# Kernel tuning notes

Hardware: AMD Instinct MI355X
Metric: run time of the kernel (lower is better)

The kernel has to match this reference:

```python
import jax, jax.numpy as jnp
import numpy as np

N = 100000
E = 3200000
NFEAT = 256
NHID = 128
NCLASS = 40
SCALE = 1.0


def setup_inputs() -> dict:
    key = jax.random.key(0)
    ks = jax.random.split(key, 8)
    x = jax.random.normal(ks[0], (N, NFEAT), dtype=jnp.float32)
    adj_row = jnp.sort(jax.random.randint(ks[1], (E,), 0, N, dtype=jnp.int32))
    adj_col = jax.random.randint(ks[2], (E,), 0, N, dtype=jnp.int32)
    adj_val = jax.random.uniform(ks[3], (E,), dtype=jnp.float32)
    # parameters (reset_parameters: weight ~ N(0,1), bias ~ N(-1,1) -> normal with mean -1? no:
    # bias.normal_(-stdv, stdv) with stdv=1 means mean=-1, std=1)
    W1 = jax.random.normal(ks[4], (NFEAT, NHID), dtype=jnp.float32)
    b1 = jax.random.normal(ks[5], (NHID,), dtype=jnp.float32) - 1.0
    W2 = jax.random.normal(ks[6], (NHID, NCLASS), dtype=jnp.float32)
    b2 = jax.random.normal(ks[7], (NCLASS,), dtype=jnp.float32) - 1.0
    return {"x": x, "adj_row": adj_row, "adj_col": adj_col, "adj_val": adj_val,
            "i": 0, "W1": W1, "b1": b1, "W2": W2, "b2": b2}


def spmm(row, col, val, dense):
    # adj @ dense where adj is sparse COO [N, N]
    gathered = val[:, None] * dense[col]          # [E, D]
    return jax.ops.segment_sum(gathered, row, num_segments=N)


def reference(x, adj_row, adj_col, adj_val, i, W1, b1, W2, b2):
    # layer 1: support = x @ W1; out = adj @ support + b1
    h = spmm(adj_row, adj_col, adj_val, x @ W1) + b1
    h = jax.nn.relu(h) * SCALE
    # dropout is identity (eval mode / training=False)
    # layer 2
    logits = spmm(adj_row, adj_col, adj_val, h @ W2) + b2
    return jax.nn.log_softmax(logits, axis=1)
```

## Files before the change

### kernel.cpp

```cpp
#include <hip/hip_runtime.h>
#include <hip/hip_bf16.h>
#include <math.h>


#define GCN_NFEAT 256
#define GCN_NHID  128
#define GCN_NCLASS 40

typedef __bf16 bf16_t;
typedef bf16_t bf16x8 __attribute__((ext_vector_type(8)));
typedef float  f32x4  __attribute__((ext_vector_type(4)));

static __device__ __forceinline__ unsigned short f2b(float f) {
    bf16_t b = (bf16_t)f;
    return *(unsigned short*)&b;
}
static __device__ __forceinline__ float blo(unsigned int u) {
    return __uint_as_float(u << 16);
}
static __device__ __forceinline__ float bhi(unsigned int u) {
    return __uint_as_float(u & 0xffff0000u);
}

__global__ __launch_bounds__(256) void k_row_ptr(
    const int* __restrict__ row, int* __restrict__ row_ptr, int n_rows, int n_edges)
{
    int r = blockIdx.x * blockDim.x + threadIdx.x;
    if (r > n_rows) return;
    int lo = 0, hi = n_edges;
    while (lo < hi) {
        int mid = (lo + hi) >> 1;
        if (row[mid] < r) lo = mid + 1; else hi = mid;
    }
    row_ptr[r] = lo;
}

__global__ __launch_bounds__(256) void k_prep_w1t(
    const float* __restrict__ w1, bf16_t* __restrict__ w1t)
{
    int idx = blockIdx.x * 256 + threadIdx.x;
    int c = idx & 127;
    int k = idx >> 7;
    w1t[(size_t)c * GCN_NFEAT + k] = (bf16_t)w1[(size_t)k * GCN_NHID + c];
}

__global__ __launch_bounds__(256) void k_prep_w2t(
    const float* __restrict__ w2, bf16_t* __restrict__ w2t)
{
    int idx = blockIdx.x * 256 + threadIdx.x;
    if (idx >= 48 * GCN_NHID) return;
    int c = idx / GCN_NHID;
    int k = idx - c * GCN_NHID;
    float v = (c < GCN_NCLASS) ? w2[(size_t)k * GCN_NCLASS + c] : 0.f;
    w2t[idx] = (bf16_t)v;
}

__global__ __launch_bounds__(256) void k_gemm1(
    const float* __restrict__ x, const bf16_t* __restrict__ w1t,
    bf16_t* __restrict__ out, int nrows)
{
    __shared__ __align__(16) bf16_t As[128][72];
    __shared__ __align__(16) bf16_t Bs[128][72];

    const int tid  = threadIdx.x;
    const int wave = tid >> 6, lane = tid & 63;
    const int wm = wave >> 1, wn = wave & 1;
    const int lm = lane & 15, quad = lane >> 4;
    const int r0 = blockIdx.x * 128;

    f32x4 acc[4][4] = {};

    for (int k0 = 0; k0 < GCN_NFEAT; k0 += 64) {
        {
            const int row = tid >> 1, half = tid & 1;
            const int gr = r0 + row;
            union { bf16_t b[32]; uint4 q[4]; } t;
            if (gr < nrows) {
                const float* p = x + (size_t)gr * GCN_NFEAT + k0 + half * 32;
#pragma unroll
                for (int i = 0; i < 8; i++) {
                    float4 v = ((const float4*)p)[i];
                    t.b[i*4+0] = (bf16_t)v.x; t.b[i*4+1] = (bf16_t)v.y;
                    t.b[i*4+2] = (bf16_t)v.z; t.b[i*4+3] = (bf16_t)v.w;
                }
            } else {
#pragma unroll
                for (int i = 0; i < 4; i++) t.q[i] = make_uint4(0,0,0,0);
            }
            uint4* dst = (uint4*)&As[row][half * 32];
#pragma unroll
            for (int i = 0; i < 4; i++) dst[i] = t.q[i];
        }
        {
            const int colc = tid >> 1, half = tid & 1;
            const uint4* src = (const uint4*)(w1t + (size_t)colc * GCN_NFEAT + k0 + half * 32);
            uint4* dst = (uint4*)&Bs[colc][half * 32];
#pragma unroll
            for (int i = 0; i < 4; i++) dst[i] = src[i];
        }
        __syncthreads();

#pragma unroll
        for (int ks = 0; ks < 2; ks++) {
            bf16x8 af[4], bfr[4];
#pragma unroll
            for (int i = 0; i < 4; i++)
                af[i] = *(const bf16x8*)&As[wm*64 + i*16 + lm][ks*32 + quad*8];
#pragma unroll
            for (int j = 0; j < 4; j++)
                bfr[j] = *(const bf16x8*)&Bs[wn*64 + j*16 + lm][ks*32 + quad*8];
#pragma unroll
            for (int i = 0; i < 4; i++)
#pragma unroll
                for (int j = 0; j < 4; j++)
                    acc[i][j] = __builtin_amdgcn_mfma_f32_16x16x32_bf16(
                        af[i], bfr[j], acc[i][j], 0, 0, 0);
        }
        __syncthreads();
    }

#pragma unroll
    for (int i = 0; i < 4; i++) {
#pragma unroll
        for (int reg = 0; reg < 4; reg++) {
            const int gr = r0 + wm*64 + i*16 + quad*4 + reg;
            if (gr < nrows) {
#pragma unroll
                for (int j = 0; j < 4; j++) {
                    const int gc = wn*64 + j*16 + lm;
                    out[(size_t)gr * GCN_NHID + gc] = (bf16_t)acc[i][j][reg];
                }
            }
        }
    }
}

__global__ __launch_bounds__(256) void k_spmm1(
    const int* __restrict__ row_ptr, const int* __restrict__ col,
    const float* __restrict__ val, const unsigned int* __restrict__ sup,
    const float* __restrict__ b1, unsigned int* __restrict__ h, int nrows)
{
    const int wid  = (blockIdx.x * blockDim.x + threadIdx.x) >> 6;
    const int lane = threadIdx.x & 63;
    if (wid >= nrows) return;
    const int e0 = row_ptr[wid];
    const int e1 = row_ptr[wid + 1];
    const int sub = lane & 15;

    float ax = 0.f, ay = 0.f;
    int e = e0;
    for (; e + 16 <= e1; e += 16) {
        const int   cv = col[e + sub];
        const float vv = val[e + sub];
#pragma unroll
        for (int j = 0; j < 16; j++) {
            const int   cj = __shfl(cv, j, 64);
            const float vj = __shfl(vv, j, 64);
            const unsigned int u = sup[(unsigned)(cj << 6) + lane];
            ax = fmaf(vj, blo(u), ax);
            ay = fmaf(vj, bhi(u), ay);
        }
    }
    for (; e < e1; e++) {
        const int c = col[e];
        const float v = val[e];
        const unsigned int u = sup[(unsigned)(c << 6) + lane];
        ax = fmaf(v, blo(u), ax);
        ay = fmaf(v, bhi(u), ay);
    }

    const float2 bb = *(const float2*)(b1 + lane * 2);
    const float ox = fmaxf(ax + bb.x, 0.f);
    const float oy = fmaxf(ay + bb.y, 0.f);
    h[(unsigned)(wid << 6) + lane] = (unsigned int)f2b(ox) | ((unsigned int)f2b(oy) << 16);
}

__global__ __launch_bounds__(256) void k_gemm2(
    const bf16_t* __restrict__ h, const bf16_t* __restrict__ w2t,
    bf16_t* __restrict__ out, int nrows)
{
    __shared__ __align__(16) bf16_t As[128][136];
    __shared__ __align__(16) bf16_t Bs[48][136];

    const int tid  = threadIdx.x;
    const int wave = tid >> 6, lane = tid & 63;
    const int lm = lane & 15, quad = lane >> 4;
    const int r0 = blockIdx.x * 128;

    {
        const int row = tid >> 1, half = tid & 1;
        const int gr = r0 + row;
        uint4* dst = (uint4*)&As[row][half * 64];
        if (gr < nrows) {
            const uint4* src = (const uint4*)(h + (size_t)gr * GCN_NHID + half * 64);
#pragma unroll
            for (int i = 0; i < 8; i++) dst[i] = src[i];
        } else {
#pragma unroll
            for (int i = 0; i < 8; i++) dst[i] = make_uint4(0,0,0,0);
        }
    }
    for (int idx = tid; idx < 48 * 16; idx += 256) {
        const int c = idx >> 4, seg = idx & 15;
        ((uint4*)&Bs[c][0])[seg] = ((const uint4*)(w2t + (size_t)c * GCN_NHID))[seg];
    }
    __syncthreads();

    f32x4 acc[2][3] = {};
#pragma unroll
    for (int ks = 0; ks < 4; ks++) {
        bf16x8 af[2], bfr[3];
#pragma unroll
        for (int i = 0; i < 2; i++)
            af[i] = *(const bf16x8*)&As[wave*32 + i*16 + lm][ks*32 + quad*8];
#pragma unroll
        for (int j = 0; j < 3; j++)
            bfr[j] = *(const bf16x8*)&Bs[j*16 + lm][ks*32 + quad*8];
#pragma unroll
        for (int i = 0; i < 2; i++)
#pragma unroll
            for (int j = 0; j < 3; j++)
                acc[i][j] = __builtin_amdgcn_mfma_f32_16x16x32_bf16(
                    af[i], bfr[j], acc[i][j], 0, 0, 0);
    }

#pragma unroll
    for (int i = 0; i < 2; i++) {
#pragma unroll
        for (int reg = 0; reg < 4; reg++) {
            const int gr = r0 + wave*32 + i*16 + quad*4 + reg;
            if (gr < nrows) {
#pragma unroll
                for (int j = 0; j < 3; j++) {
                    const int gc = j*16 + lm;
                    if (gc < GCN_NCLASS)
                        out[(size_t)gr * GCN_NCLASS + gc] = (bf16_t)acc[i][j][reg];
                }
            }
        }
    }
}

__global__ __launch_bounds__(256) void k_spmm2_lsm(
    const int* __restrict__ row_ptr, const int* __restrict__ col,
    const float* __restrict__ val, const unsigned int* __restrict__ sup2,
    const float* __restrict__ b2, float* __restrict__ out, int nrows)
{
    const int wid  = (blockIdx.x * blockDim.x + threadIdx.x) >> 6;
    const int lane = threadIdx.x & 63;
    const int g    = lane / 20;
    const int li   = lane - g * 20;
    const int r    = wid * 3 + g;
    const bool active = (g < 3) && (r < nrows);

    int e0 = 0, e1 = 0;
    if (active) { e0 = row_ptr[r]; e1 = row_ptr[r + 1]; }

    float ax = 0.f, ay = 0.f;
    int e = e0;
    for (; e + 3 < e1; e += 4) {
        const int c0 = col[e],   c1 = col[e+1], c2 = col[e+2], c3 = col[e+3];
        const float v0 = val[e], v1 = val[e+1], v2 = val[e+2], v3 = val[e+3];
        const unsigned int u0 = sup2[(unsigned)(c0 * 20) + li];
        const unsigned int u1 = sup2[(unsigned)(c1 * 20) + li];
        const unsigned int u2 = sup2[(unsigned)(c2 * 20) + li];
        const unsigned int u3 = sup2[(unsigned)(c3 * 20) + li];
        ax = fmaf(v0, blo(u0), ax); ay = fmaf(v0, bhi(u0), ay);
        ax = fmaf(v1, blo(u1), ax); ay = fmaf(v1, bhi(u1), ay);
        ax = fmaf(v2, blo(u2), ax); ay = fmaf(v2, bhi(u2), ay);
        ax = fmaf(v3, blo(u3), ax); ay = fmaf(v3, bhi(u3), ay);
    }
    for (; e < e1; e++) {
        const unsigned int u = sup2[(unsigned)(col[e] * 20) + li];
        const float v = val[e];
        ax = fmaf(v, blo(u), ax); ay = fmaf(v, bhi(u), ay);
    }

    float l0 = -INFINITY, l1 = -INFINITY;
    if (active) {
        l0 = ax + b2[li * 2];
        l1 = ay + b2[li * 2 + 1];
    }

    float m = fmaxf(l0, l1);
#pragma unroll
    for (int off = 16; off >= 1; off >>= 1) {
        const float t = __shfl_down(m, off, 64);
        if (li + off < 20) m = fmaxf(m, t);
    }
    m = __shfl(m, g * 20, 64);

    float s = active ? (__expf(l0 - m) + __expf(l1 - m)) : 0.f;
#pragma unroll
    for (int off = 16; off >= 1; off >>= 1) {
        const float t = __shfl_down(s, off, 64);
        if (li + off < 20) s += t;
    }
    s = __shfl(s, g * 20, 64);

    if (active) {
        const float lse = m + __logf(s);
        float* p = out + (size_t)r * GCN_NCLASS + li * 2;
        p[0] = l0 - lse;
        p[1] = l1 - lse;
    }
}

extern "C" void kernel_launch(void* const* d_in, const int* in_sizes, int n_in,
                              void* d_out, int out_size, void* d_ws, size_t ws_size,
                              hipStream_t stream)
{
    const float* x       = (const float*)d_in[0];
    const int*   adj_row = (const int*)  d_in[1];
    const int*   adj_col = (const int*)  d_in[2];
    const float* adj_val = (const float*)d_in[3];
    const float* W1 = (const float*)d_in[5];
    const float* b1 = (const float*)d_in[6];
    const float* W2 = (const float*)d_in[7];
    const float* b2 = (const float*)d_in[8];
    float* out = (float*)d_out;

    const int N = in_sizes[0] / GCN_NFEAT;
    const int E = in_sizes[1];

    char* ws = (char*)d_ws;
    size_t off = 0;
    int* row_ptr = (int*)(ws + off);
    off += (((size_t)(N + 1) * sizeof(int)) + 1023) & ~(size_t)1023;
    bf16_t* w1t = (bf16_t*)(ws + off);
    off += ((size_t)GCN_NHID * GCN_NFEAT * 2 + 1023) & ~(size_t)1023;
    bf16_t* w2t = (bf16_t*)(ws + off);
    off += ((size_t)48 * GCN_NHID * 2 + 1023) & ~(size_t)1023;
    bf16_t* sup1 = (bf16_t*)(ws + off);
    off += ((size_t)N * GCN_NHID * 2 + 1023) & ~(size_t)1023;
    bf16_t* h = (bf16_t*)(ws + off);
    bf16_t* sup2 = sup1;

    k_row_ptr<<<(N + 1 + 255) / 256, 256, 0, stream>>>(adj_row, row_ptr, N, E);
    k_prep_w1t<<<GCN_NHID * GCN_NFEAT / 256, 256, 0, stream>>>(W1, w1t);
    k_prep_w2t<<<(48 * GCN_NHID + 255) / 256, 256, 0, stream>>>(W2, w2t);
    k_gemm1<<<(N + 127) / 128, 256, 0, stream>>>(x, w1t, sup1, N);
    k_spmm1<<<(N + 3) / 4, 256, 0, stream>>>(row_ptr, adj_col, adj_val,
                                             (const unsigned int*)sup1, b1,
                                             (unsigned int*)h, N);
    k_gemm2<<<(N + 127) / 128, 256, 0, stream>>>(h, w2t, sup2, N);
    const int nw2 = (N + 2) / 3;
    k_spmm2_lsm<<<(nw2 + 3) / 4, 256, 0, stream>>>(row_ptr, adj_col, adj_val,
                                                   (const unsigned int*)sup2, b2, out, N);
}
```

Before: 417.3 us.

## Merge prep kernels, use 16-byte gathers in spmm1, add nontemporal loads

Merges the row-pointer and weight-transpose launches into one kernel. Rewrites spmm1 so each wave handles four edges at once: each 16-lane quarter gathers a full 256-byte bf16 row with 16-byte loads, and partial sums are combined with cross-lane shuffles. Adds nontemporal loads for x in gemm1 and for col/val in the spmm kernels, and an 8-way unrolled loop in spmm2. The aim is to cut launch overhead and gather instruction count and to improve memory-level parallelism, at the cost of extra shuffle reductions and more complex tail handling.

Measured after the change: 426.0 us. 1.02x slower.

```diff
diff --git a/kernel.cpp b/kernel.cpp
--- a/kernel.cpp
+++ b/kernel.cpp
@@ -10,6 +10,7 @@
 typedef __bf16 bf16_t;
 typedef bf16_t bf16x8 __attribute__((ext_vector_type(8)));
 typedef float  f32x4  __attribute__((ext_vector_type(4)));
+typedef float  f32x4e __attribute__((ext_vector_type(4)));
 
 static __device__ __forceinline__ unsigned short f2b(float f) {
     bf16_t b = (bf16_t)f;
@@ -22,37 +23,35 @@
     return __uint_as_float(u & 0xffff0000u);
 }
 
-__global__ __launch_bounds__(256) void k_row_ptr(
-    const int* __restrict__ row, int* __restrict__ row_ptr, int n_rows, int n_edges)
-{
-    int r = blockIdx.x * blockDim.x + threadIdx.x;
-    if (r > n_rows) return;
-    int lo = 0, hi = n_edges;
-    while (lo < hi) {
-        int mid = (lo + hi) >> 1;
-        if (row[mid] < r) lo = mid + 1; else hi = mid;
-    }
-    row_ptr[r] = lo;
-}
-
-__global__ __launch_bounds__(256) void k_prep_w1t(
-    const float* __restrict__ w1, bf16_t* __restrict__ w1t)
-{
-    int idx = blockIdx.x * 256 + threadIdx.x;
-    int c = idx & 127;
-    int k = idx >> 7;
-    w1t[(size_t)c * GCN_NFEAT + k] = (bf16_t)w1[(size_t)k * GCN_NHID + c];
-}
-
-__global__ __launch_bounds__(256) void k_prep_w2t(
-    const float* __restrict__ w2, bf16_t* __restrict__ w2t)
-{
-    int idx = blockIdx.x * 256 + threadIdx.x;
-    if (idx >= 48 * GCN_NHID) return;
-    int c = idx / GCN_NHID;
-    int k = idx - c * GCN_NHID;
-    float v = (c < GCN_NCLASS) ? w2[(size_t)k * GCN_NCLASS + c] : 0.f;
-    w2t[idx] = (bf16_t)v;
+__global__ __launch_bounds__(256) void k_prep(
+    const int* __restrict__ row, int* __restrict__ row_ptr,
+    const float* __restrict__ w1, bf16_t* __restrict__ w1t,
+    const float* __restrict__ w2, bf16_t* __restrict__ w2t,
+    int n_rows, int n_edges, int rb)
+{
+    const int b = blockIdx.x;
+    if (b < rb) {
+        int r = b * 256 + threadIdx.x;
+        if (r > n_rows) return;
+        int lo = 0, hi = n_edges;
+        while (lo < hi) {
+            int mid = (lo + hi) >> 1;
+            if (row[mid] < r) lo = mid + 1; else hi = mid;
+        }
+        row_ptr[r] = lo;
+    } else if (b < rb + 128) {
+        int idx = (b - rb) * 256 + threadIdx.x;
+        int c = idx & 127;
+        int k = idx >> 7;
+        w1t[(size_t)c * GCN_NFEAT + k] = (bf16_t)w1[(size_t)k * GCN_NHID + c];
+    } else {
+        int idx = (b - rb - 128) * 256 + threadIdx.x;
+        if (idx >= 48 * GCN_NHID) return;
+        int c = idx / GCN_NHID;
+        int k = idx - c * GCN_NHID;
+        float v = (c < GCN_NCLASS) ? w2[(size_t)k * GCN_NCLASS + c] : 0.f;
+        w2t[idx] = (bf16_t)v;
+    }
 }
 
 __global__ __launch_bounds__(256) void k_gemm1(
@@ -76,10 +75,10 @@
             const int gr = r0 + row;
             union { bf16_t b[32]; uint4 q[4]; } t;
             if (gr < nrows) {
-                const float* p = x + (size_t)gr * GCN_NFEAT + k0 + half * 32;
+                const f32x4e* p = (const f32x4e*)(x + (size_t)gr * GCN_NFEAT + k0 + half * 32);
 #pragma unroll
                 for (int i = 0; i < 8; i++) {
-                    float4 v = ((const float4*)p)[i];
+                    f32x4e v = __builtin_nontemporal_load(p + i);
                     t.b[i*4+0] = (bf16_t)v.x; t.b[i*4+1] = (bf16_t)v.y;
                     t.b[i*4+2] = (bf16_t)v.z; t.b[i*4+3] = (bf16_t)v.w;
                 }
@@ -135,44 +134,105 @@
     }
 }
 
+#define S1_FENCE(U) asm volatile("" : "+v"(U.x), "+v"(U.y), "+v"(U.z), "+v"(U.w));
+#define S1_FMA(U, V)                                   \
+    a0 = fmaf(V, blo(U.x), a0); a1 = fmaf(V, bhi(U.x), a1); \
+    a2 = fmaf(V, blo(U.y), a2); a3 = fmaf(V, bhi(U.y), a3); \
+    a4 = fmaf(V, blo(U.z), a4); a5 = fmaf(V, bhi(U.z), a5); \
+    a6 = fmaf(V, blo(U.w), a6); a7 = fmaf(V, bhi(U.w), a7);
+
 __global__ __launch_bounds__(256) void k_spmm1(
     const int* __restrict__ row_ptr, const int* __restrict__ col,
-    const float* __restrict__ val, const unsigned int* __restrict__ sup,
+    const float* __restrict__ val, const bf16_t* __restrict__ sup,
     const float* __restrict__ b1, unsigned int* __restrict__ h, int nrows)
 {
     const int wid  = (blockIdx.x * blockDim.x + threadIdx.x) >> 6;
     const int lane = threadIdx.x & 63;
     if (wid >= nrows) return;
-    const int e0 = row_ptr[wid];
-    const int e1 = row_ptr[wid + 1];
-    const int sub = lane & 15;
-
-    float ax = 0.f, ay = 0.f;
-    int e = e0;
-    for (; e + 16 <= e1; e += 16) {
-        const int   cv = col[e + sub];
-        const float vv = val[e + sub];
-#pragma unroll
-        for (int j = 0; j < 16; j++) {
-            const int   cj = __shfl(cv, j, 64);
-            const float vj = __shfl(vv, j, 64);
-            const unsigned int u = sup[(unsigned)(cj << 6) + lane];
-            ax = fmaf(vj, blo(u), ax);
-            ay = fmaf(vj, bhi(u), ay);
-        }
-    }
-    for (; e < e1; e++) {
-        const int c = col[e];
-        const float v = val[e];
-        const unsigned int u = sup[(unsigned)(c << 6) + lane];
-        ax = fmaf(v, blo(u), ax);
-        ay = fmaf(v, bhi(u), ay);
-    }
-
-    const float2 bb = *(const float2*)(b1 + lane * 2);
-    const float ox = fmaxf(ax + bb.x, 0.f);
-    const float oy = fmaxf(ay + bb.y, 0.f);
-    h[(unsigned)(wid << 6) + lane] = (unsigned int)f2b(ox) | ((unsigned int)f2b(oy) << 16);
+    const int q = lane >> 4;
+    const int f = lane & 15;
+    const int e0 = __builtin_amdgcn_readfirstlane(row_ptr[wid]);
+    const int e1 = __builtin_amdgcn_readfirstlane(row_ptr[wid + 1]);
+    const int n  = e1 - e0;
+    const char* supb = (const char*)sup;
+    const int fo = f * 16;
+
+    float a0=0.f,a1=0.f,a2=0.f,a3=0.f,a4=0.f,a5=0.f,a6=0.f,a7=0.f;
+
+    int base = 0;
+    for (; base + 16 <= n; base += 16) {
+        const int i0 = e0 + base + q;
+        const int   c0 = __builtin_nontemporal_load(col + i0);
+        const float v0 = __builtin_nontemporal_load(val + i0);
+        const int   c1 = __builtin_nontemporal_load(col + i0 + 4);
+        const float v1 = __builtin_nontemporal_load(val + i0 + 4);
+        const int   c2 = __builtin_nontemporal_load(col + i0 + 8);
+        const float v2 = __builtin_nontemporal_load(val + i0 + 8);
+        const int   c3 = __builtin_nontemporal_load(col + i0 + 12);
+        const float v3 = __builtin_nontemporal_load(val + i0 + 12);
+        uint4 u0 = *(const uint4*)(supb + (((size_t)(unsigned)c0) << 8) + fo);
+        uint4 u1 = *(const uint4*)(supb + (((size_t)(unsigned)c1) << 8) + fo);
+        uint4 u2 = *(const uint4*)(supb + (((size_t)(unsigned)c2) << 8) + fo);
+        uint4 u3 = *(const uint4*)(supb + (((size_t)(unsigned)c3) << 8) + fo);
+        S1_FENCE(u0) S1_FMA(u0, v0)
+        S1_FENCE(u1) S1_FMA(u1, v1)
+        S1_FENCE(u2) S1_FMA(u2, v2)
+        S1_FENCE(u3) S1_FMA(u3, v3)
+    }
+    const int rem = n - base;
+    if (rem > 0) {
+        const int elast = e1 - 1;
+        uint4 t0, t1, t2, t3;
+        float w0 = 0.f, w1 = 0.f, w2 = 0.f, w3 = 0.f;
+        {
+            int gi = e0 + base + q; if (gi > elast) gi = elast;
+            const int c = col[gi]; w0 = (q < rem) ? val[gi] : 0.f;
+            t0 = *(const uint4*)(supb + (((size_t)(unsigned)c) << 8) + fo);
+        }
+        if (rem > 4) {
+            int gi = e0 + base + 4 + q; if (gi > elast) gi = elast;
+            const int c = col[gi]; w1 = (4 + q < rem) ? val[gi] : 0.f;
+            t1 = *(const uint4*)(supb + (((size_t)(unsigned)c) << 8) + fo);
+        }
+        if (rem > 8) {
+            int gi = e0 + base + 8 + q; if (gi > elast) gi = elast;
+            const int c = col[gi]; w2 = (8 + q < rem) ? val[gi] : 0.f;
+            t2 = *(const uint4*)(supb + (((size_t)(unsigned)c) << 8) + fo);
+        }
+        if (rem > 12) {
+            int gi = e0 + base + 12 + q; if (gi > elast) gi = elast;
+            const int c = col[gi]; w3 = (12 + q < rem) ? val[gi] : 0.f;
+            t3 = *(const uint4*)(supb + (((size_t)(unsigned)c) << 8) + fo);
+        }
+        { S1_FENCE(t0) S1_FMA(t0, w0) }
+        if (rem > 4)  { S1_FENCE(t1) S1_FMA(t1, w1) }
+        if (rem > 8)  { S1_FENCE(t2) S1_FMA(t2, w2) }
+        if (rem > 12) { S1_FENCE(t3) S1_FMA(t3, w3) }
+    }
+
+    a0 += __shfl_xor(a0, 16, 64); a1 += __shfl_xor(a1, 16, 64);
+    a2 += __shfl_xor(a2, 16, 64); a3 += __shfl_xor(a3, 16, 64);
+    a4 += __shfl_xor(a4, 16, 64); a5 += __shfl_xor(a5, 16, 64);
+    a6 += __shfl_xor(a6, 16, 64); a7 += __shfl_xor(a7, 16, 64);
+    a0 += __shfl_xor(a0, 32, 64); a1 += __shfl_xor(a1, 32, 64);
+    a2 += __shfl_xor(a2, 32, 64); a3 += __shfl_xor(a3, 32, 64);
+    a4 += __shfl_xor(a4, 32, 64); a5 += __shfl_xor(a5, 32, 64);
+    a6 += __shfl_xor(a6, 32, 64); a7 += __shfl_xor(a7, 32, 64);
+
+    if (q == 0) {
+        const float4 ba = *(const float4*)(b1 + f * 8);
+        const float4 bc = *(const float4*)(b1 + f * 8 + 4);
+        const float o0 = fmaxf(a0 + ba.x, 0.f), o1 = fmaxf(a1 + ba.y, 0.f);
+        const float o2 = fmaxf(a2 + ba.z, 0.f), o3 = fmaxf(a3 + ba.w, 0.f);
+        const float o4 = fmaxf(a4 + bc.x, 0.f), o5 = fmaxf(a5 + bc.y, 0.f);
+        const float o6 = fmaxf(a6 + bc.z, 0.f), o7 = fmaxf(a7 + bc.w, 0.f);
+        uint4 pk;
+        pk.x = (unsigned)f2b(o0) | ((unsigned)f2b(o1) << 16);
+        pk.y = (unsigned)f2b(o2) | ((unsigned)f2b(o3) << 16);
+        pk.z = (unsigned)f2b(o4) | ((unsigned)f2b(o5) << 16);
+        pk.w = (unsigned)f2b(o6) | ((unsigned)f2b(o7) << 16);
+        *(uint4*)(h + ((unsigned)wid << 6) + (f << 2)) = pk;
+    }
 }
 
 __global__ __launch_bounds__(256) void k_gemm2(
@@ -258,6 +318,40 @@
 
     float ax = 0.f, ay = 0.f;
     int e = e0;
+    for (; e + 7 < e1; e += 8) {
+        const int c0 = __builtin_nontemporal_load(col + e);
+        const int c1 = __builtin_nontemporal_load(col + e + 1);
+        const int c2 = __builtin_nontemporal_load(col + e + 2);
+        const int c3 = __builtin_nontemporal_load(col + e + 3);
+        const int c4 = __builtin_nontemporal_load(col + e + 4);
+        const int c5 = __builtin_nontemporal_load(col + e + 5);
+        const int c6 = __builtin_nontemporal_load(col + e + 6);
+        const int c7 = __builtin_nontemporal_load(col + e + 7);
+        const float v0 = __builtin_nontemporal_load(val + e);
+        const float v1 = __builtin_nontemporal_load(val + e + 1);
+        const float v2 = __builtin_nontemporal_load(val + e + 2);
+        const float v3 = __builtin_nontemporal_load(val + e + 3);
+        const float v4 = __builtin_nontemporal_load(val + e + 4);
+        const float v5 = __builtin_nontemporal_load(val + e + 5);
+        const float v6 = __builtin_nontemporal_load(val + e + 6);
+        const float v7 = __builtin_nontemporal_load(val + e + 7);
+        const unsigned int u0 = sup2[(unsigned)(c0 * 20) + li];
+        const unsigned int u1 = sup2[(unsigned)(c1 * 20) + li];
+        const unsigned int u2 = sup2[(unsigned)(c2 * 20) + li];
+        const unsigned int u3 = sup2[(unsigned)(c3 * 20) + li];
+        const unsigned int u4 = sup2[(unsigned)(c4 * 20) + li];
+        const unsigned int u5 = sup2[(unsigned)(c5 * 20) + li];
+        const unsigned int u6 = sup2[(unsigned)(c6 * 20) + li];
+        const unsigned int u7 = sup2[(unsigned)(c7 * 20) + li];
+        ax = fmaf(v0, blo(u0), ax); ay = fmaf(v0, bhi(u0), ay);
+        ax = fmaf(v1, blo(u1), ax); ay = fmaf(v1, bhi(u1), ay);
+        ax = fmaf(v2, blo(u2), ax); ay = fmaf(v2, bhi(u2), ay);
+        ax = fmaf(v3, blo(u3), ax); ay = fmaf(v3, bhi(u3), ay);
+        ax = fmaf(v4, blo(u4), ax); ay = fmaf(v4, bhi(u4), ay);
+        ax = fmaf(v5, blo(u5), ax); ay = fmaf(v5, bhi(u5), ay);
+        ax = fmaf(v6, blo(u6), ax); ay = fmaf(v6, bhi(u6), ay);
+        ax = fmaf(v7, blo(u7), ax); ay = fmaf(v7, bhi(u7), ay);
+    }
     for (; e + 3 < e1; e += 4) {
         const int c0 = col[e],   c1 = col[e+1], c2 = col[e+2], c3 = col[e+3];
         const float v0 = val[e], v1 = val[e+1], v2 = val[e+2], v3 = val[e+3];
@@ -336,13 +430,12 @@
     bf16_t* h = (bf16_t*)(ws + off);
     bf16_t* sup2 = sup1;
 
-    k_row_ptr<<<(N + 1 + 255) / 256, 256, 0, stream>>>(adj_row, row_ptr, N, E);
-    k_prep_w1t<<<GCN_NHID * GCN_NFEAT / 256, 256, 0, stream>>>(W1, w1t);
-    k_prep_w2t<<<(48 * GCN_NHID + 255) / 256, 256, 0, stream>>>(W2, w2t);
+    const int rb = (N + 1 + 255) / 256;
+    k_prep<<<rb + 128 + 24, 256, 0, stream>>>(adj_row, row_ptr, W1, w1t, W2, w2t,
+                                              N, E, rb);
     k_gemm1<<<(N + 127) / 128, 256, 0, stream>>>(x, w1t, sup1, N);
     k_spmm1<<<(N + 3) / 4, 256, 0, stream>>>(row_ptr, adj_col, adj_val,
-                                             (const unsigned int*)sup1, b1,
-                                             (unsigned int*)h, N);
+                                             sup1, b1, (unsigned int*)h, N);
     k_gemm2<<<(N + 127) / 128, 256, 0, stream>>>(h, w2t, sup2, N);
     const int nw2 = (N + 2) / 3;
     k_spmm2_lsm<<<(nw2 + 3) / 4, 256, 0, stream>>>(row_ptr, adj_col, adj_val,
```
